# Optimization experiments

Measured on AMD Instinct MI355X. Metric: run time of the kernel, lower is better.

The kernel has to match this reference:

```python
import jax, jax.numpy as jnp
import numpy as np
from jax import lax

T, B, H, NF, FS = 512, 128, 512, 128, 5  # max_seq_len, batch, hidden, num_filters, filter_size


def setup_inputs() -> dict:
    key = jax.random.key(0)
    ks = jax.random.split(key, 16)
    inp = {
        "encoder_output": jax.random.normal(ks[0], (T, B, H), dtype=jnp.float32),
        "lengths": jax.random.randint(ks[1], (B,), 1, T + 1, dtype=jnp.int64 if jax.config.jax_enable_x64 else jnp.int32),
    }
    for w in range(1, FS + 1):
        inp[f"conv_w{w}"] = jax.random.normal(ks[1 + w], (NF, 1, H, w), dtype=jnp.float32) * 0.02
        inp[f"conv_b{w}"] = jnp.zeros((NF,), dtype=jnp.float32)
    inp["fc1_w"] = jax.random.normal(ks[12], (100, FS * NF), dtype=jnp.float32) * 0.05
    inp["fc1_b"] = jnp.zeros((100,), dtype=jnp.float32)
    inp["fc2_w"] = jax.random.normal(ks[13], (1, 100), dtype=jnp.float32) * 0.1
    inp["fc2_b"] = jnp.zeros((1,), dtype=jnp.float32)
    return inp


def _raw_reshape(x, L):
    # Faithful to torch .contiguous().view(1,1,H,-1) on a [L,H] slice:
    # row-major flatten of first L rows, reshaped to [H, L], zero-padded to [H, T].
    flat = x.reshape(-1)                       # [T*H]
    h = jnp.arange(H)[:, None]                 # [H,1]
    l = jnp.arange(T)[None, :]                 # [1,T]
    return jnp.where(l < L, flat[h * L + l], 0.0)  # [H,T]


def reference(encoder_output, lengths,
              conv_w1, conv_b1, conv_w2, conv_b2, conv_w3, conv_b3,
              conv_w4, conv_b4, conv_w5, conv_b5,
              fc1_w, fc1_b, fc2_w, fc2_b):
    # encoder_output: [T, B, H]; per-sample raw reshape to [H, T] (length-dependent)
    X = jax.vmap(_raw_reshape, in_axes=(1, 0))(encoder_output, lengths)  # [B,H,T]
    X4 = X[:, None, :, :]                                               # [B,1,H,T]
    Leff = jnp.maximum(lengths, FS)  # torch code zero-pads width to >= filter_size
    conv_ws = [conv_w1, conv_w2, conv_w3, conv_w4, conv_w5]
    conv_bs = [conv_b1, conv_b2, conv_b3, conv_b4, conv_b5]
    pools = []
    for w in range(1, FS + 1):
        out = lax.conv_general_dilated(
            X4, conv_ws[w - 1], window_strides=(1, 1), padding='VALID',
            dimension_numbers=('NCHW', 'OIHW', 'NCHW'))          # [B,NF,1,T-w+1]
        r = jax.nn.relu(out[:, :, 0, :] + conv_bs[w - 1][None, :, None])  # [B,NF,Tw]
        tpos = jnp.arange(T - w + 1)
        valid = tpos[None, :] < (Leff - w + 1)[:, None]          # [B,Tw]
        r = jnp.where(valid[:, None, :], r, 0.0)                 # relu>=0, so 0 is safe for max
        pools.append(r.max(axis=2))                              # [B,NF]
    feat = jnp.concatenate(pools, axis=1)                        # [B,FS*NF]
    fc1 = feat @ fc1_w.T + fc1_b
    fc2 = fc1 @ fc2_w.T + fc2_b
    probs = jax.nn.sigmoid(fc2)                                  # [B,1]
    return probs[:, None, :]                                     # [B,1,1] == torch.stack of [1,1]
```

## Files before the change

kernel.cpp:

```cpp
#include <hip/hip_runtime.h>
#include <hip/hip_bf16.h>

#define TT 512
#define BB 128
#define HH 512
#define NFC 128

typedef short v8s __attribute__((ext_vector_type(8)));
typedef float v4f __attribute__((ext_vector_type(4)));

__device__ __forceinline__ unsigned short f2bf(float x) {
    unsigned u = __float_as_uint(x);
    unsigned r = (u + 0x7fffu + ((u >> 16) & 1u)) >> 16;
    return (unsigned short)r;
}

__global__ void prep_all(const float* __restrict__ enc, const int* __restrict__ lengths,
                         unsigned short* __restrict__ Xg,
                         const float* __restrict__ w1, const float* __restrict__ w2,
                         const float* __restrict__ w3, const float* __restrict__ w4,
                         const float* __restrict__ w5, unsigned short* __restrict__ Wg,
                         float* __restrict__ pools,
                         const float* __restrict__ fc1w, const float* __restrict__ fc1b,
                         const float* __restrict__ fc2w, const float* __restrict__ fc2b,
                         float* __restrict__ v) {
    int blk = blockIdx.x;
    int tid = threadIdx.x;
    if (blk < 8192) {
        __shared__ float tile[64 * 65];
        int b = blk >> 6;
        int lc = (blk >> 3) & 7;
        int hc = blk & 7;
        int L = lengths[b];
        int Leff = L > 5 ? L : 5;
        int l0 = lc * 64, h0 = hc * 64;
        if ((l0 & ~127) >= Leff) return;
        int lx = tid & 63;
        int hq = tid >> 6;
        #pragma unroll
        for (int r = 0; r < 16; ++r) {
            int hl = hq * 16 + r;
            int l = l0 + lx;
            float val = 0.f;
            if (l < L) {
                int i = (h0 + hl) * L + l;
                val = enc[(i >> 9) * (BB * HH) + b * HH + (i & 511)];
            }
            tile[hl * 65 + lx] = val;
        }
        __syncthreads();
        int hg = tid & 15;
        #pragma unroll
        for (int r = 0; r < 4; ++r) {
            int lloc = (tid >> 4) + r * 16;
            int n = b * 512 + l0 + lloc;
            ushort4 pk;
            pk.x = f2bf(tile[(hg * 4 + 0) * 65 + lloc]);
            pk.y = f2bf(tile[(hg * 4 + 1) * 65 + lloc]);
            pk.z = f2bf(tile[(hg * 4 + 2) * 65 + lloc]);
            pk.w = f2bf(tile[(hg * 4 + 3) * 65 + lloc]);
            *(ushort4*)&Xg[n * 512 + h0 + hg * 4] = pk;
        }
    } else if (blk < 12288) {
        int idx = (blk - 8192) * 256 + tid;
        int s = idx >> 9, h = idx & 511;
        int f = s >> 4, sl = s & 15;
        float val = 0.f;
        if (sl < 15) {
            int w, j;
            if (sl < 1)       { w = 1; j = sl; }
            else if (sl < 3)  { w = 2; j = sl - 1; }
            else if (sl < 6)  { w = 3; j = sl - 3; }
            else if (sl < 10) { w = 4; j = sl - 6; }
            else              { w = 5; j = sl - 10; }
            const float* wp = (w == 1) ? w1 : (w == 2) ? w2 : (w == 3) ? w3 : (w == 4) ? w4 : w5;
            val = wp[f * (HH * w) + h * w + j];
        }
        Wg[idx] = f2bf(val);
    } else if (blk < 12608) {
        int i = (blk - 12288) * 256 + tid;
        if (i < BB * 5 * NFC) pools[i] = 0.f;
    } else {
        for (int k = tid; k < 640; k += 256) {
            float s = 0.f;
            for (int o = 0; o < 100; ++o) s += fc2w[o] * fc1w[o * 640 + k];
            v[k] = s;
        }
        if (tid == 0) {
            float c = fc2b[0];
            for (int o = 0; o < 100; ++o) c += fc2w[o] * fc1b[o];
            v[640] = c;
        }
    }
}

__global__ __launch_bounds__(256, 4)
void conv_gemm(const unsigned short* __restrict__ Wg, const unsigned short* __restrict__ Xg,
               const int* __restrict__ lengths,
               const float* __restrict__ cb1, const float* __restrict__ cb2,
               const float* __restrict__ cb3, const float* __restrict__ cb4,
               const float* __restrict__ cb5,
               float* __restrict__ pools, float* __restrict__ strips) {
    __shared__ __align__(16) char smem[64 * 129 * 4];
    unsigned short* ldsA = (unsigned short*)smem;
    unsigned short* ldsB = (unsigned short*)(smem + 16384);
    float* Gs = (float*)smem;

    int bi = blockIdx.x;
    int b = bi >> 6;
    int mtile = (bi >> 2) & 15;
    int tt = bi & 3;
    int L = lengths[b];
    int Leff = L > 5 ? L : 5;
    if (tt * 128 >= Leff) return;

    int tid = threadIdx.x;
    int wid = tid >> 6, lane = tid & 63;
    int wm = wid >> 1, wn = wid & 1;
    int llo = lane & 15, quad = lane >> 4;

    int m0 = mtile * 128;
    int nb0 = b * 512 + tt * 128;

    v4f acc[4][4];
    #pragma unroll
    for (int i = 0; i < 4; ++i)
        #pragma unroll
        for (int j = 0; j < 4; ++j) acc[i][j] = v4f{0.f, 0.f, 0.f, 0.f};

    int srow8 = lane >> 3;
    int gchunk = (lane & 7) ^ srow8;
    const unsigned short* gA = Wg + (m0 + wid * 32 + srow8) * 512 + gchunk * 8;
    const unsigned short* gB = Xg + (nb0 + wid * 32 + srow8) * 512 + gchunk * 8;

    #pragma unroll 1
    for (int kt = 0; kt < 8; ++kt) {
        int ko = kt * 64;
        #pragma unroll
        for (int q = 0; q < 4; ++q) {
            __builtin_amdgcn_global_load_lds(
                (const __attribute__((address_space(1))) unsigned int*)(gA + q * (8 * 512) + ko),
                (__attribute__((address_space(3))) unsigned int*)&ldsA[(wid * 32 + q * 8) * 64],
                16, 0, 0);
            __builtin_amdgcn_global_load_lds(
                (const __attribute__((address_space(1))) unsigned int*)(gB + q * (8 * 512) + ko),
                (__attribute__((address_space(3))) unsigned int*)&ldsB[(wid * 32 + q * 8) * 64],
                16, 0, 0);
        }
        __syncthreads();
        #pragma unroll
        for (int kh = 0; kh < 2; ++kh) {
            int pk = (((kh * 4 + quad) ^ (llo & 7))) * 8;
            v8s Af[4], Bf[4];
            #pragma unroll
            for (int mi = 0; mi < 4; ++mi)
                Af[mi] = *(const v8s*)&ldsA[(wm * 64 + mi * 16 + llo) * 64 + pk];
            #pragma unroll
            for (int ni = 0; ni < 4; ++ni)
                Bf[ni] = *(const v8s*)&ldsB[(wn * 64 + ni * 16 + llo) * 64 + pk];
            #pragma unroll
            for (int mi = 0; mi < 4; ++mi)
                #pragma unroll
                for (int ni = 0; ni < 4; ++ni)
                    acc[mi][ni] = __builtin_amdgcn_mfma_f32_16x16x32_bf16(Af[mi], Bf[ni], acc[mi][ni], 0, 0, 0);
        }
        __syncthreads();
    }

    const int basew[6] = {0, 0, 1, 3, 6, 10};
    long sbase = (long)(((b * 4 + tt) * 16 + mtile) * 128) * 8;

    #pragma unroll 1
    for (int phase = 0; phase < 2; ++phase) {
        if (wm == phase) {
            #pragma unroll
            for (int mi = 0; mi < 4; ++mi)
                #pragma unroll
                for (int ni = 0; ni < 4; ++ni)
                    #pragma unroll
                    for (int r = 0; r < 4; ++r)
                        Gs[(mi * 16 + quad * 4 + r) * 129 + wn * 64 + ni * 16 + llo] = acc[mi][ni][r];
        }
        __syncthreads();
        {
            int row = tid >> 3, c = tid & 7;
            int col = (c < 4) ? c : (120 + c);
            #pragma unroll
            for (int rr = 0; rr < 2; ++rr) {
                int r2 = row + rr * 32;
                strips[sbase + (phase * 64 + r2) * 8 + c] = Gs[r2 * 129 + col];
            }
        }
        {
            int fl = wid;
            int f = mtile * 8 + phase * 4 + fl;
            #pragma unroll
            for (int w = 1; w <= 5; ++w) {
                float bias = (w == 1 ? cb1 : w == 2 ? cb2 : w == 3 ? cb3 : w == 4 ? cb4 : cb5)[f];
                int limt = 128 - w;
                int limv = Leff - w + 1 - tt * 128;
                float vmax = -1.f;
                #pragma unroll
                for (int half = 0; half < 2; ++half) {
                    int t = half * 64 + lane;
                    if (t <= limt && t < limv) {
                        float s = 0.f;
                        #pragma unroll
                        for (int j = 0; j < w; ++j)
                            s += Gs[(fl * 16 + basew[w] + j) * 129 + t + j];
                        s += bias;
                        s = fmaxf(s, 0.f);
                        vmax = fmaxf(vmax, s);
                    }
                }
                #pragma unroll
                for (int off = 32; off >= 1; off >>= 1)
                    vmax = fmaxf(vmax, __shfl_xor(vmax, off));
                if (lane == 0 && vmax >= 0.f)
                    atomicMax((int*)&pools[(b * 5 + (w - 1)) * NFC + f], __float_as_int(vmax));
            }
        }
        __syncthreads();
    }
}

__global__ void cleanup(const float* __restrict__ strips, const int* __restrict__ lengths,
                        const float* __restrict__ cb2, const float* __restrict__ cb3,
                        const float* __restrict__ cb4, const float* __restrict__ cb5,
                        float* __restrict__ pools) {
    int idx = blockIdx.x * 64 + threadIdx.x;
    if (idx >= 16384) return;
    int b = idx >> 7;
    int mtile = (idx >> 3) & 15;
    int fl = idx & 7;
    int L = lengths[b];
    int Leff = L > 5 ? L : 5;
    int f = mtile * 8 + fl;
    const int basew[6] = {0, 0, 1, 3, 6, 10};
    for (int t2 = 0; t2 < 3; ++t2) {
        if (Leff < t2 * 128 + 129) break;
        const float* s0 = strips + (long)(((b * 4 + t2) * 16 + mtile) * 128) * 8;
        const float* s1 = strips + (long)(((b * 4 + t2 + 1) * 16 + mtile) * 128) * 8;
        #pragma unroll
        for (int w = 2; w <= 5; ++w) {
            float bias = (w == 2 ? cb2 : w == 3 ? cb3 : w == 4 ? cb4 : cb5)[f];
            float best = -1.f;
            for (int t = 129 - w; t <= 127; ++t) {
                int tg = t2 * 128 + t;
                if (tg >= Leff - w + 1) continue;
                float s = 0.f;
                #pragma unroll
                for (int j = 0; j < w; ++j) {
                    int c = t + j;
                    int row = fl * 16 + basew[w] + j;
                    s += (c <= 127) ? s0[row * 8 + (c - 120)] : s1[row * 8 + (c - 128)];
                }
                s += bias;
                s = fmaxf(s, 0.f);
                best = fmaxf(best, s);
            }
            if (best >= 0.f)
                atomicMax((int*)&pools[(b * 5 + (w - 1)) * NFC + f], __float_as_int(best));
        }
    }
}

__global__ void head(const float* __restrict__ pools, const float* __restrict__ v,
                     float* __restrict__ out) {
    int b = blockIdx.x;
    int tid = threadIdx.x;
    float s = 0.f;
    for (int k = tid; k < 640; k += 256) s += pools[b * 640 + k] * v[k];
    __shared__ float red[256];
    red[tid] = s;
    __syncthreads();
    for (int st = 128; st; st >>= 1) {
        if (tid < st) red[tid] += red[tid + st];
        __syncthreads();
    }
    if (tid == 0) out[b] = 1.f / (1.f + expf(-(red[0] + v[640])));
}

extern "C" void kernel_launch(void* const* d_in, const int* in_sizes, int n_in,
                              void* d_out, int out_size, void* d_ws, size_t ws_size,
                              hipStream_t stream) {
    const float* enc  = (const float*)d_in[0];
    const int* lens   = (const int*)d_in[1];
    const float* w1   = (const float*)d_in[2];
    const float* b1   = (const float*)d_in[3];
    const float* w2   = (const float*)d_in[4];
    const float* b2   = (const float*)d_in[5];
    const float* w3   = (const float*)d_in[6];
    const float* b3   = (const float*)d_in[7];
    const float* w4   = (const float*)d_in[8];
    const float* b4   = (const float*)d_in[9];
    const float* w5   = (const float*)d_in[10];
    const float* b5   = (const float*)d_in[11];
    const float* fc1w = (const float*)d_in[12];
    const float* fc1b = (const float*)d_in[13];
    const float* fc2w = (const float*)d_in[14];
    const float* fc2b = (const float*)d_in[15];
    float* out = (float*)d_out;

    unsigned short* Xg = (unsigned short*)d_ws;
    unsigned short* Wg = Xg + 33554432;
    float* strips = (float*)(Wg + 1048576);
    float* pools  = strips + 8388608;
    float* vbuf   = pools + 81920;

    prep_all<<<12609, 256, 0, stream>>>(enc, lens, Xg, w1, w2, w3, w4, w5, Wg, pools,
                                        fc1w, fc1b, fc2w, fc2b, vbuf);
    conv_gemm<<<8192, 256, 0, stream>>>(Wg, Xg, lens, b1, b2, b3, b4, b5, pools, strips);
    cleanup<<<256, 64, 0, stream>>>(strips, lens, b2, b3, b4, b5, pools);
    head<<<128, 256, 0, stream>>>(pools, vbuf, out);
}
```

Measured before the change: 419.6 us.

## Use overlapping N-tiles with 256-row M tiles and drop cleanup kernel

The conv GEMM now uses 256x128 output tiles with overlapping time windows (stride 124) so each tile computes all window sums locally. This removes the strips buffer and the separate boundary cleanup kernel. K-step is halved to 32 with a new LDS swizzle, and the occupancy hint in the launch bounds is dropped. Overlap adds a small amount of redundant GEMM work and higher register pressure from the 8x4 accumulator tiles.

```diff
diff --git a/kernel.cpp b/kernel.cpp
--- a/kernel.cpp
+++ b/kernel.cpp
@@ -34,7 +34,7 @@
         int L = lengths[b];
         int Leff = L > 5 ? L : 5;
         int l0 = lc * 64, h0 = hc * 64;
-        if ((l0 & ~127) >= Leff) return;
+        if (l0 >= Leff + 127) return;
         int lx = tid & 63;
         int hq = tid >> 6;
         #pragma unroll
@@ -94,124 +94,110 @@
     }
 }
 
-__global__ __launch_bounds__(256, 4)
+__global__ __launch_bounds__(256)
 void conv_gemm(const unsigned short* __restrict__ Wg, const unsigned short* __restrict__ Xg,
                const int* __restrict__ lengths,
                const float* __restrict__ cb1, const float* __restrict__ cb2,
                const float* __restrict__ cb3, const float* __restrict__ cb4,
                const float* __restrict__ cb5,
-               float* __restrict__ pools, float* __restrict__ strips) {
-    __shared__ __align__(16) char smem[64 * 129 * 4];
+               float* __restrict__ pools) {
+    __shared__ __align__(16) char smem[24576];
     unsigned short* ldsA = (unsigned short*)smem;
     unsigned short* ldsB = (unsigned short*)(smem + 16384);
     float* Gs = (float*)smem;
 
     int bi = blockIdx.x;
-    int b = bi >> 6;
-    int mtile = (bi >> 2) & 15;
-    int tt = bi & 3;
+    int tt = bi % 5;
+    int r5 = bi / 5;
+    int mt = r5 & 7;
+    int b  = r5 >> 3;
+    int n0 = tt * 124 - ((tt >> 2) * 112);
     int L = lengths[b];
     int Leff = L > 5 ? L : 5;
-    if (tt * 128 >= Leff) return;
+    if (n0 >= Leff) return;
 
     int tid = threadIdx.x;
     int wid = tid >> 6, lane = tid & 63;
     int wm = wid >> 1, wn = wid & 1;
     int llo = lane & 15, quad = lane >> 4;
-
-    int m0 = mtile * 128;
-    int nb0 = b * 512 + tt * 128;
-
-    v4f acc[4][4];
+    int psw = quad ^ ((llo >> 1) & 3);
+
+    int m0 = mt * 256;
+    int nb0 = b * 512 + n0;
+
+    v4f acc[8][4];
     #pragma unroll
-    for (int i = 0; i < 4; ++i)
+    for (int i = 0; i < 8; ++i)
         #pragma unroll
         for (int j = 0; j < 4; ++j) acc[i][j] = v4f{0.f, 0.f, 0.f, 0.f};
 
-    int srow8 = lane >> 3;
-    int gchunk = (lane & 7) ^ srow8;
-    const unsigned short* gA = Wg + (m0 + wid * 32 + srow8) * 512 + gchunk * 8;
-    const unsigned short* gB = Xg + (nb0 + wid * 32 + srow8) * 512 + gchunk * 8;
+    int srow = lane >> 2;
+    int gchunk = (lane & 3) ^ ((lane >> 3) & 3);
+    const unsigned short* gA = Wg + (m0 + wid * 64 + srow) * 512 + gchunk * 8;
+    const unsigned short* gB = Xg + (nb0 + wid * 32 + srow) * 512 + gchunk * 8;
 
     #pragma unroll 1
-    for (int kt = 0; kt < 8; ++kt) {
-        int ko = kt * 64;
-        #pragma unroll
-        for (int q = 0; q < 4; ++q) {
+    for (int kt = 0; kt < 16; ++kt) {
+        int ko = kt * 32;
+        #pragma unroll
+        for (int q = 0; q < 4; ++q)
             __builtin_amdgcn_global_load_lds(
-                (const __attribute__((address_space(1))) unsigned int*)(gA + q * (8 * 512) + ko),
-                (__attribute__((address_space(3))) unsigned int*)&ldsA[(wid * 32 + q * 8) * 64],
+                (const __attribute__((address_space(1))) unsigned int*)(gA + q * (16 * 512) + ko),
+                (__attribute__((address_space(3))) unsigned int*)&ldsA[(wid * 64 + q * 16) * 32],
                 16, 0, 0);
+        #pragma unroll
+        for (int q = 0; q < 2; ++q)
             __builtin_amdgcn_global_load_lds(
-                (const __attribute__((address_space(1))) unsigned int*)(gB + q * (8 * 512) + ko),
-                (__attribute__((address_space(3))) unsigned int*)&ldsB[(wid * 32 + q * 8) * 64],
+                (const __attribute__((address_space(1))) unsigned int*)(gB + q * (16 * 512) + ko),
+                (__attribute__((address_space(3))) unsigned int*)&ldsB[(wid * 32 + q * 16) * 32],
                 16, 0, 0);
-        }
-        __syncthreads();
-        #pragma unroll
-        for (int kh = 0; kh < 2; ++kh) {
-            int pk = (((kh * 4 + quad) ^ (llo & 7))) * 8;
-            v8s Af[4], Bf[4];
-            #pragma unroll
-            for (int mi = 0; mi < 4; ++mi)
-                Af[mi] = *(const v8s*)&ldsA[(wm * 64 + mi * 16 + llo) * 64 + pk];
+        __syncthreads();
+        v8s Af[8], Bf[4];
+        #pragma unroll
+        for (int mi = 0; mi < 8; ++mi)
+            Af[mi] = *(const v8s*)&ldsA[(wm * 128 + mi * 16 + llo) * 32 + psw * 8];
+        #pragma unroll
+        for (int ni = 0; ni < 4; ++ni)
+            Bf[ni] = *(const v8s*)&ldsB[(wn * 64 + ni * 16 + llo) * 32 + psw * 8];
+        #pragma unroll
+        for (int mi = 0; mi < 8; ++mi)
             #pragma unroll
             for (int ni = 0; ni < 4; ++ni)
-                Bf[ni] = *(const v8s*)&ldsB[(wn * 64 + ni * 16 + llo) * 64 + pk];
+                acc[mi][ni] = __builtin_amdgcn_mfma_f32_16x16x32_bf16(Af[mi], Bf[ni], acc[mi][ni], 0, 0, 0);
+        __syncthreads();
+    }
+
+    const int basew[6] = {0, 0, 1, 3, 6, 10};
+
+    #pragma unroll 1
+    for (int p = 0; p < 8; ++p) {
+        if (wm == (p >> 2)) {
+            int mb = (p & 3) * 2;
             #pragma unroll
-            for (int mi = 0; mi < 4; ++mi)
-                #pragma unroll
-                for (int ni = 0; ni < 4; ++ni)
-                    acc[mi][ni] = __builtin_amdgcn_mfma_f32_16x16x32_bf16(Af[mi], Bf[ni], acc[mi][ni], 0, 0, 0);
-        }
-        __syncthreads();
-    }
-
-    const int basew[6] = {0, 0, 1, 3, 6, 10};
-    long sbase = (long)(((b * 4 + tt) * 16 + mtile) * 128) * 8;
-
-    #pragma unroll 1
-    for (int phase = 0; phase < 2; ++phase) {
-        if (wm == phase) {
-            #pragma unroll
-            for (int mi = 0; mi < 4; ++mi)
+            for (int mi2 = 0; mi2 < 2; ++mi2)
                 #pragma unroll
                 for (int ni = 0; ni < 4; ++ni)
                     #pragma unroll
                     for (int r = 0; r < 4; ++r)
-                        Gs[(mi * 16 + quad * 4 + r) * 129 + wn * 64 + ni * 16 + llo] = acc[mi][ni][r];
+                        Gs[(mi2 * 16 + quad * 4 + r) * 129 + wn * 64 + ni * 16 + llo] = acc[mb + mi2][ni][r];
         }
         __syncthreads();
         {
-            int row = tid >> 3, c = tid & 7;
-            int col = (c < 4) ? c : (120 + c);
-            #pragma unroll
-            for (int rr = 0; rr < 2; ++rr) {
-                int r2 = row + rr * 32;
-                strips[sbase + (phase * 64 + r2) * 8 + c] = Gs[r2 * 129 + col];
-            }
-        }
-        {
-            int fl = wid;
-            int f = mtile * 8 + phase * 4 + fl;
+            int fg = wid & 1, half = wid >> 1;
+            int f = mt * 16 + p * 2 + fg;
+            int t = half * 64 + lane;
             #pragma unroll
             for (int w = 1; w <= 5; ++w) {
                 float bias = (w == 1 ? cb1 : w == 2 ? cb2 : w == 3 ? cb3 : w == 4 ? cb4 : cb5)[f];
-                int limt = 128 - w;
-                int limv = Leff - w + 1 - tt * 128;
+                int limv = Leff - w + 1 - n0;
                 float vmax = -1.f;
-                #pragma unroll
-                for (int half = 0; half < 2; ++half) {
-                    int t = half * 64 + lane;
-                    if (t <= limt && t < limv) {
-                        float s = 0.f;
-                        #pragma unroll
-                        for (int j = 0; j < w; ++j)
-                            s += Gs[(fl * 16 + basew[w] + j) * 129 + t + j];
-                        s += bias;
-                        s = fmaxf(s, 0.f);
-                        vmax = fmaxf(vmax, s);
-                    }
+                if (t <= 128 - w && t < limv) {
+                    float s = 0.f;
+                    #pragma unroll
+                    for (int j = 0; j < w; ++j)
+                        s += Gs[(fg * 16 + basew[w] + j) * 129 + t + j];
+                    s += bias;
+                    vmax = fmaxf(s, 0.f);
                 }
                 #pragma unroll
                 for (int off = 32; off >= 1; off >>= 1)
@@ -221,47 +207,6 @@
             }
         }
         __syncthreads();
-    }
-}
-
-__global__ void cleanup(const float* __restrict__ strips, const int* __restrict__ lengths,
-                        const float* __restrict__ cb2, const float* __restrict__ cb3,
-                        const float* __restrict__ cb4, const float* __restrict__ cb5,
-                        float* __restrict__ pools) {
-    int idx = blockIdx.x * 64 + threadIdx.x;
-    if (idx >= 16384) return;
-    int b = idx >> 7;
-    int mtile = (idx >> 3) & 15;
-    int fl = idx & 7;
-    int L = lengths[b];
-    int Leff = L > 5 ? L : 5;
-    int f = mtile * 8 + fl;
-    const int basew[6] = {0, 0, 1, 3, 6, 10};
-    for (int t2 = 0; t2 < 3; ++t2) {
-        if (Leff < t2 * 128 + 129) break;
-        const float* s0 = strips + (long)(((b * 4 + t2) * 16 + mtile) * 128) * 8;
-        const float* s1 = strips + (long)(((b * 4 + t2 + 1) * 16 + mtile) * 128) * 8;
-        #pragma unroll
-        for (int w = 2; w <= 5; ++w) {
-            float bias = (w == 2 ? cb2 : w == 3 ? cb3 : w == 4 ? cb4 : cb5)[f];
-            float best = -1.f;
-            for (int t = 129 - w; t <= 127; ++t) {
-                int tg = t2 * 128 + t;
-                if (tg >= Leff - w + 1) continue;
-                float s = 0.f;
-                #pragma unroll
-                for (int j = 0; j < w; ++j) {
-                    int c = t + j;
-                    int row = fl * 16 + basew[w] + j;
-                    s += (c <= 127) ? s0[row * 8 + (c - 120)] : s1[row * 8 + (c - 128)];
-                }
-                s += bias;
-                s = fmaxf(s, 0.f);
-                best = fmaxf(best, s);
-            }
-            if (best >= 0.f)
-                atomicMax((int*)&pools[(b * 5 + (w - 1)) * NFC + f], __float_as_int(best));
-        }
     }
 }
 
@@ -304,13 +249,11 @@
 
     unsigned short* Xg = (unsigned short*)d_ws;
     unsigned short* Wg = Xg + 33554432;
-    float* strips = (float*)(Wg + 1048576);
-    float* pools  = strips + 8388608;
+    float* pools  = (float*)(Wg + 1048576);
     float* vbuf   = pools + 81920;
 
     prep_all<<<12609, 256, 0, stream>>>(enc, lens, Xg, w1, w2, w3, w4, w5, Wg, pools,
                                         fc1w, fc1b, fc2w, fc2b, vbuf);
-    conv_gemm<<<8192, 256, 0, stream>>>(Wg, Xg, lens, b1, b2, b3, b4, b5, pools, strips);
-    cleanup<<<256, 64, 0, stream>>>(strips, lens, b2, b3, b4, b5, pools);
+    conv_gemm<<<5120, 256, 0, stream>>>(Wg, Xg, lens, b1, b2, b3, b4, b5, pools);
     head<<<128, 256, 0, stream>>>(pools, vbuf, out);
 }
```

New measurement: 1.295 ms. +208.6%, slower.
